# Kernel optimization log

Hardware: AMD Instinct MI355X
Metric: run time of the kernel (lower is better)

Reference implementation:

```python
import jax, jax.numpy as jnp
import numpy as np
from jax.scipy.special import logsumexp

T, B, D, L = 1024, 32, 768, 48
NEG = jnp.float32(-1e20)


def setup_inputs() -> dict:
    key = jax.random.key(0)
    ks = jax.random.split(key, 10)
    feats = jax.random.normal(ks[0], (T, B, D), jnp.float32)
    # tags: True = label disallowed at this position (partial annotation mask)
    tags = jax.random.uniform(ks[1], (T, B, L)) < 0.3
    lens = jax.random.randint(ks[2], (B,), T // 2, T + 1)
    W = jax.random.normal(ks[3], (D, L), jnp.float32) * 0.02
    b = jnp.zeros((L,), jnp.float32)
    base = jnp.float32(1.0 / L)
    begin_transition = jnp.full((L,), base) + 0.01 * jax.random.normal(ks[4], (L,), jnp.float32)
    transitions = jnp.full((L, L), base) + 0.01 * jax.random.normal(ks[5], (L, L), jnp.float32)
    end_transition = jnp.full((L,), base) + 0.01 * jax.random.normal(ks[6], (L,), jnp.float32)
    begin_constraints = jax.random.uniform(ks[7], (L,)) < 0.2
    end_constraints = jax.random.uniform(ks[8], (L,)) < 0.2
    transition_constraints = jax.random.uniform(ks[9], (L, L)) < 0.2
    return {
        "feats": feats, "tags": tags, "lens": lens,
        "W": W, "b": b,
        "begin_transition": begin_transition, "transitions": transitions,
        "end_transition": end_transition,
        "begin_constraints": begin_constraints, "end_constraints": end_constraints,
        "transition_constraints": transition_constraints,
    }


def _crf_logZ(emissions, begin, trans, end, tag_mask, lens):
    """Forward algorithm over [T,B,L] emissions; tag_mask True = disallowed.
    Returns log partition per batch element, read out at step lens-1."""
    fs0 = emissions[0] + begin[None, :]              # [B, L]
    fs0 = jnp.where(tag_mask[0], NEG, fs0)

    def step(prev, xs):
        em_t, m_t = xs
        # new[b, j] = logsumexp_k(prev[b, k] + trans[j, k]) + em_t[b, j]
        new = logsumexp(prev[:, None, :] + trans[None, :, :], axis=-1) + em_t
        new = jnp.where(m_t, NEG, new)
        return new, new

    _, ys = jax.lax.scan(step, fs0, (emissions[1:], tag_mask[1:]))
    all_fs = jnp.concatenate([fs0[None], ys], axis=0)        # [T, B, L]
    last = all_fs[lens - 1, jnp.arange(lens.shape[0])]       # [B, L]
    return logsumexp(last + end[None, :], axis=-1)           # [B]


def reference(feats, tags, lens, W, b, begin_transition, transitions,
              end_transition, begin_constraints, end_constraints,
              transition_constraints):
    # feature2labels (Dropout is identity in eval)
    emissions = jnp.einsum('tbd,dl->tbl', feats, W) + b      # [T, B, L]
    no_mask = jnp.zeros_like(tags)

    # forward_alg: unconstrained partition function
    fwd = _crf_logZ(emissions, begin_transition, transitions,
                    end_transition, no_mask, lens)

    # partial_score: constrained params + gold tag masking
    begin_m = jnp.where(begin_constraints, NEG, begin_transition)
    trans_m = jnp.where(transition_constraints, NEG, transitions)
    end_m = jnp.where(end_constraints, NEG, end_transition)
    par = _crf_logZ(emissions, begin_m, trans_m, end_m, tags, lens)

    # criterion per batch element (sum over batch = original scalar loss)
    return fwd - par                                          # [B]
```

## Files before the change

kernel.cpp:

```cpp
#include <hip/hip_runtime.h>

#define T_ 1024
#define B_ 32
#define D_ 768
#define L_ 48
#define TB_ (T_ * B_)

typedef __attribute__((ext_vector_type(4))) float f32x4;

__global__ __launch_bounds__(256) void emis_gemm(
    const float* __restrict__ feats, const float* __restrict__ W,
    const float* __restrict__ bias, float* __restrict__ E) {
  __shared__ float fbuf[128 * 64];
  __shared__ float wbuf[48 * 68];
  const int tid = threadIdx.x;
  const int wv = tid >> 6;
  const int lane = tid & 63;
  const int cg = tid & 7;
  const int rg = tid >> 3;
  const int c0 = cg * 6;
  const int rowbase = blockIdx.x * 128;
  const int r7 = rg & 7;

  float acc[4][6];
#pragma unroll
  for (int i = 0; i < 4; i++)
#pragma unroll
    for (int c = 0; c < 6; c++) acc[i][c] = 0.f;

  for (int kc = 0; kc < D_; kc += 64) {
    __syncthreads();

#pragma unroll
    for (int inst = 0; inst < 8; inst++) {
      const int rowstart = wv * 32 + inst * 4;
      const int r = rowstart + (lane >> 4);
      const int slot = lane & 15;
      const int gch = slot ^ (r & 7);
      const float* g = feats + (size_t)(rowbase + r) * D_ + kc + gch * 4;
      float* l = fbuf + rowstart * 64;
      __builtin_amdgcn_global_load_lds(
          (const __attribute__((address_space(1))) uint32_t*)g,
          (__attribute__((address_space(3))) uint32_t*)l, 16, 0, 0);
    }

#pragma unroll
    for (int i = 0; i < 12; i++) {
      const int idx = tid + i * 256;
      const int ko = idx / 48;
      const int j = idx - ko * 48;
      wbuf[j * 68 + ko] = W[(kc + ko) * L_ + j];
    }

    __syncthreads();

#pragma unroll 4
    for (int k4 = 0; k4 < 16; k4++) {
      float4 fv[4];
      float4 wv4[6];
      const int sch = (k4 ^ r7) << 2;
#pragma unroll
      for (int i = 0; i < 4; i++)
        fv[i] = *(const float4*)(fbuf + (rg + 32 * i) * 64 + sch);
#pragma unroll
      for (int c = 0; c < 6; c++)
        wv4[c] = *(const float4*)(wbuf + (c0 + c) * 68 + k4 * 4);
#pragma unroll
      for (int i = 0; i < 4; i++) {
#pragma unroll
        for (int c = 0; c < 6; c++) {
          acc[i][c] = fmaf(fv[i].x, wv4[c].x, acc[i][c]);
          acc[i][c] = fmaf(fv[i].y, wv4[c].y, acc[i][c]);
          acc[i][c] = fmaf(fv[i].z, wv4[c].z, acc[i][c]);
          acc[i][c] = fmaf(fv[i].w, wv4[c].w, acc[i][c]);
        }
      }
    }
  }

#pragma unroll
  for (int i = 0; i < 4; i++) {
    float* dst = E + (size_t)(rowbase + rg + 32 * i) * L_ + c0;
#pragma unroll
    for (int c = 0; c < 6; c += 2) {
      float2 v;
      v.x = __expf(acc[i][c + 0] + bias[c0 + c + 0]);
      v.y = __expf(acc[i][c + 1] + bias[c0 + c + 1]);
      *(float2*)(dst + c) = v;
    }
  }
}

__global__ __launch_bounds__(128) void crf_scan(
    const float* __restrict__ E, const int* __restrict__ tags,
    const int* __restrict__ lens, const float* __restrict__ begin,
    const float* __restrict__ trans, const float* __restrict__ endt,
    const int* __restrict__ bc, const int* __restrict__ ec,
    const int* __restrict__ tc, float* __restrict__ out) {
  __shared__ __align__(16) float sbuf[2][2][64];
  __shared__ float lzbuf[2];
  const int b = blockIdx.x;
  const int wv = threadIdx.x >> 6;
  const int lane = threadIdx.x & 63;
  const bool act = lane < L_;
  const bool par = (wv == 1);
  const int len = lens[b];
  const int stride = B_ * L_;
  const int base = b * L_ + (act ? lane : 0);

  float P[L_];
#pragma unroll
  for (int k = 0; k < L_; k++) P[k] = 0.f;
  if (act) {
#pragma unroll
    for (int k = 0; k < L_; k++) {
      float v = __expf(trans[lane * L_ + k]);
      if (par && tc[lane * L_ + k]) v = 0.f;
      P[k] = v;
    }
  }

  float a = 0.f;
  if (act) {
    a = E[base] * __expf(begin[lane]);
    if (par && (bc[lane] || tags[base])) a = 0.f;
  }
  float logacc = 0.f;
  float pend = 1.f;

  sbuf[wv][0][lane] = a;

  auto step = [&](int i, float ev, int tg, bool resc) {
    const float evp = ev * pend;
    pend = 1.f;
    const f32x4* src = (const f32x4*)sbuf[wv][i & 1];
    float s0 = 0.f, s1 = 0.f, s2 = 0.f, s3 = 0.f;
#pragma unroll
    for (int c = 0; c < 12; c++) {
      const f32x4 q = src[c];
      s0 = fmaf(q.x, P[4 * c + 0], s0);
      s1 = fmaf(q.y, P[4 * c + 1], s1);
      s2 = fmaf(q.z, P[4 * c + 2], s2);
      s3 = fmaf(q.w, P[4 * c + 3], s3);
    }
    float u = ((s0 + s1) + (s2 + s3)) * evp;
    if (tg) u = 0.f;
    a = u;
    sbuf[wv][(i + 1) & 1][lane] = u;
    if (resc) {
      float m = u;
#pragma unroll
      for (int off = 32; off; off >>= 1) m = fmaxf(m, __shfl_xor(m, off, 64));
      m = fmaxf(m, 1e-30f);
      logacc += __logf(m);
      pend = 1.f / m;
    }
  };

  float e8[8];
  int tg8[8];
#pragma unroll
  for (int i = 0; i < 8; i++) {
    e8[i] = E[(size_t)(1 + i) * stride + base];
    tg8[i] = par ? tags[(size_t)(1 + i) * stride + base] : 0;
  }

  int t = 1;
  for (; t + 8 <= len; t += 8) {
    float p8[8];
    int q8[8];
#pragma unroll
    for (int i = 0; i < 8; i++) {
      int tt = t + 8 + i;
      tt = (tt < len) ? tt : (len - 1);
      p8[i] = E[(size_t)tt * stride + base];
      q8[i] = par ? tags[(size_t)tt * stride + base] : 0;
    }
#pragma unroll
    for (int i = 0; i < 8; i++) step(i, e8[i], tg8[i], i == 7);
#pragma unroll
    for (int i = 0; i < 8; i++) { e8[i] = p8[i]; tg8[i] = q8[i]; }
  }
#pragma unroll
  for (int i = 0; i < 8; i++) {
    if (t + i < len) step(i, e8[i], tg8[i], false);
  }

  float z = 0.f;
  if (act) {
    float ez = __expf(endt[lane]);
    if (par && ec[lane]) ez = 0.f;
    z = a * ez;
  }
#pragma unroll
  for (int off = 32; off; off >>= 1) z += __shfl_xor(z, off, 64);
  if (lane == 0) lzbuf[wv] = logacc + __logf(pend) + __logf(z);
  __syncthreads();
  if (threadIdx.x == 0) out[b] = lzbuf[0] - lzbuf[1];
}

extern "C" void kernel_launch(void* const* d_in, const int* in_sizes, int n_in,
                              void* d_out, int out_size, void* d_ws,
                              size_t ws_size, hipStream_t stream) {
  (void)in_sizes; (void)n_in; (void)out_size; (void)ws_size;
  const float* feats = (const float*)d_in[0];
  const int* tags = (const int*)d_in[1];
  const int* lens = (const int*)d_in[2];
  const float* W = (const float*)d_in[3];
  const float* bias = (const float*)d_in[4];
  const float* begin = (const float*)d_in[5];
  const float* trans = (const float*)d_in[6];
  const float* endt = (const float*)d_in[7];
  const int* bc = (const int*)d_in[8];
  const int* ec = (const int*)d_in[9];
  const int* tc = (const int*)d_in[10];

  float* E = (float*)d_ws;
  float* out = (float*)d_out;

  emis_gemm<<<dim3(TB_ / 128), dim3(256), 0, stream>>>(feats, W, bias, E);
  crf_scan<<<dim3(B_), dim3(128), 0, stream>>>(E, tags, lens, begin, trans,
                                               endt, bc, ec, tc, out);
}
```

Measured before the change: 494.6 us.

## Double-buffer GEMM tiles and compute CRF rescale max from LDS without shuffles

The emission GEMM now double-buffers the feats and W tiles in LDS, prefetching the next k-chunk while computing the current one, so only one barrier per chunk remains. In the CRF scan, the rescale max is taken from the shared state vector already read during the matvec, which removes the cross-lane shuffle reduction from the serial dependency chain. The unroll drops from 8 to 4 steps with a rescale every 8 steps. LDS use doubles and the rescale now normalizes by the previous state's max instead of the new one, which changes numerics slightly.

```diff
diff --git a/kernel.cpp b/kernel.cpp
--- a/kernel.cpp
+++ b/kernel.cpp
@@ -8,11 +8,11 @@
 
 typedef __attribute__((ext_vector_type(4))) float f32x4;
 
-__global__ __launch_bounds__(256) void emis_gemm(
+__global__ __launch_bounds__(256, 1) void emis_gemm(
     const float* __restrict__ feats, const float* __restrict__ W,
     const float* __restrict__ bias, float* __restrict__ E) {
-  __shared__ float fbuf[128 * 64];
-  __shared__ float wbuf[48 * 68];
+  __shared__ float fbuf[2][128 * 64];
+  __shared__ float wbuf[2][48 * 68];
   const int tid = threadIdx.x;
   const int wv = tid >> 6;
   const int lane = tid & 63;
@@ -21,6 +21,17 @@
   const int c0 = cg * 6;
   const int rowbase = blockIdx.x * 128;
   const int r7 = rg & 7;
+  const int r_in = lane >> 4;
+  const int slot = lane & 15;
+
+  int woff[12];
+#pragma unroll
+  for (int i = 0; i < 12; i++) {
+    const int idx = tid + i * 256;
+    const int ko = idx / 48;
+    const int j = idx - ko * 48;
+    woff[i] = j * 68 + ko;
+  }
 
   float acc[4][6];
 #pragma unroll
@@ -28,32 +39,49 @@
 #pragma unroll
     for (int c = 0; c < 6; c++) acc[i][c] = 0.f;
 
-  for (int kc = 0; kc < D_; kc += 64) {
-    __syncthreads();
-
+  float wr[12];
+
+  {
+#pragma unroll
+    for (int i = 0; i < 12; i++) wr[i] = W[tid + i * 256];
 #pragma unroll
     for (int inst = 0; inst < 8; inst++) {
       const int rowstart = wv * 32 + inst * 4;
-      const int r = rowstart + (lane >> 4);
-      const int slot = lane & 15;
+      const int r = rowstart + r_in;
       const int gch = slot ^ (r & 7);
-      const float* g = feats + (size_t)(rowbase + r) * D_ + kc + gch * 4;
-      float* l = fbuf + rowstart * 64;
+      const float* g = feats + (size_t)(rowbase + r) * D_ + gch * 4;
+      float* l = &fbuf[0][rowstart * 64];
       __builtin_amdgcn_global_load_lds(
           (const __attribute__((address_space(1))) uint32_t*)g,
           (__attribute__((address_space(3))) uint32_t*)l, 16, 0, 0);
     }
-
-#pragma unroll
-    for (int i = 0; i < 12; i++) {
-      const int idx = tid + i * 256;
-      const int ko = idx / 48;
-      const int j = idx - ko * 48;
-      wbuf[j * 68 + ko] = W[(kc + ko) * L_ + j];
-    }
-
+#pragma unroll
+    for (int i = 0; i < 12; i++) wbuf[0][woff[i]] = wr[i];
+  }
+
+  for (int c = 0; c < 12; c++) {
+    const int cur = c & 1;
     __syncthreads();
 
+    if (c < 11) {
+      const int kc2 = (c + 1) * 64;
+#pragma unroll
+      for (int i = 0; i < 12; i++) wr[i] = W[kc2 * L_ + tid + i * 256];
+#pragma unroll
+      for (int inst = 0; inst < 8; inst++) {
+        const int rowstart = wv * 32 + inst * 4;
+        const int r = rowstart + r_in;
+        const int gch = slot ^ (r & 7);
+        const float* g = feats + (size_t)(rowbase + r) * D_ + kc2 + gch * 4;
+        float* l = &fbuf[cur ^ 1][rowstart * 64];
+        __builtin_amdgcn_global_load_lds(
+            (const __attribute__((address_space(1))) uint32_t*)g,
+            (__attribute__((address_space(3))) uint32_t*)l, 16, 0, 0);
+      }
+    }
+
+    const float* fb = fbuf[cur];
+    const float* wb = wbuf[cur];
 #pragma unroll 4
     for (int k4 = 0; k4 < 16; k4++) {
       float4 fv[4];
@@ -61,37 +89,42 @@
       const int sch = (k4 ^ r7) << 2;
 #pragma unroll
       for (int i = 0; i < 4; i++)
-        fv[i] = *(const float4*)(fbuf + (rg + 32 * i) * 64 + sch);
-#pragma unroll
-      for (int c = 0; c < 6; c++)
-        wv4[c] = *(const float4*)(wbuf + (c0 + c) * 68 + k4 * 4);
+        fv[i] = *(const float4*)(fb + (rg + 32 * i) * 64 + sch);
+#pragma unroll
+      for (int cc = 0; cc < 6; cc++)
+        wv4[cc] = *(const float4*)(wb + (c0 + cc) * 68 + k4 * 4);
 #pragma unroll
       for (int i = 0; i < 4; i++) {
 #pragma unroll
-        for (int c = 0; c < 6; c++) {
-          acc[i][c] = fmaf(fv[i].x, wv4[c].x, acc[i][c]);
-          acc[i][c] = fmaf(fv[i].y, wv4[c].y, acc[i][c]);
-          acc[i][c] = fmaf(fv[i].z, wv4[c].z, acc[i][c]);
-          acc[i][c] = fmaf(fv[i].w, wv4[c].w, acc[i][c]);
+        for (int cc = 0; cc < 6; cc++) {
+          acc[i][cc] = fmaf(fv[i].x, wv4[cc].x, acc[i][cc]);
+          acc[i][cc] = fmaf(fv[i].y, wv4[cc].y, acc[i][cc]);
+          acc[i][cc] = fmaf(fv[i].z, wv4[cc].z, acc[i][cc]);
+          acc[i][cc] = fmaf(fv[i].w, wv4[cc].w, acc[i][cc]);
         }
       }
     }
+
+    if (c < 11) {
+#pragma unroll
+      for (int i = 0; i < 12; i++) wbuf[cur ^ 1][woff[i]] = wr[i];
+    }
   }
 
 #pragma unroll
   for (int i = 0; i < 4; i++) {
     float* dst = E + (size_t)(rowbase + rg + 32 * i) * L_ + c0;
 #pragma unroll
-    for (int c = 0; c < 6; c += 2) {
+    for (int cc = 0; cc < 6; cc += 2) {
       float2 v;
-      v.x = __expf(acc[i][c + 0] + bias[c0 + c + 0]);
-      v.y = __expf(acc[i][c + 1] + bias[c0 + c + 1]);
-      *(float2*)(dst + c) = v;
+      v.x = __expf(acc[i][cc + 0] + bias[c0 + cc + 0]);
+      v.y = __expf(acc[i][cc + 1] + bias[c0 + cc + 1]);
+      *(float2*)(dst + cc) = v;
     }
   }
 }
 
-__global__ __launch_bounds__(128) void crf_scan(
+__global__ __launch_bounds__(128, 1) void crf_scan(
     const float* __restrict__ E, const int* __restrict__ tags,
     const int* __restrict__ lens, const float* __restrict__ begin,
     const float* __restrict__ trans, const float* __restrict__ endt,
@@ -126,64 +159,73 @@
     if (par && (bc[lane] || tags[base])) a = 0.f;
   }
   float logacc = 0.f;
-  float pend = 1.f;
 
   sbuf[wv][0][lane] = a;
 
   auto step = [&](int i, float ev, int tg, bool resc) {
-    const float evp = ev * pend;
-    pend = 1.f;
     const f32x4* src = (const f32x4*)sbuf[wv][i & 1];
     float s0 = 0.f, s1 = 0.f, s2 = 0.f, s3 = 0.f;
+    f32x4 mx = {0.f, 0.f, 0.f, 0.f};
 #pragma unroll
     for (int c = 0; c < 12; c++) {
       const f32x4 q = src[c];
+      if (resc) {
+        mx.x = fmaxf(mx.x, q.x);
+        mx.y = fmaxf(mx.y, q.y);
+        mx.z = fmaxf(mx.z, q.z);
+        mx.w = fmaxf(mx.w, q.w);
+      }
       s0 = fmaf(q.x, P[4 * c + 0], s0);
       s1 = fmaf(q.y, P[4 * c + 1], s1);
       s2 = fmaf(q.z, P[4 * c + 2], s2);
       s3 = fmaf(q.w, P[4 * c + 3], s3);
     }
+    float evp = ev;
+    if (resc) {
+      float m = fmaxf(fmaxf(mx.x, mx.y), fmaxf(mx.z, mx.w));
+      m = fmaxf(m, 1e-30f);
+      logacc += __logf(m);
+      evp = ev * (1.f / m);
+    }
     float u = ((s0 + s1) + (s2 + s3)) * evp;
     if (tg) u = 0.f;
     a = u;
     sbuf[wv][(i + 1) & 1][lane] = u;
-    if (resc) {
-      float m = u;
-#pragma unroll
-      for (int off = 32; off; off >>= 1) m = fmaxf(m, __shfl_xor(m, off, 64));
-      m = fmaxf(m, 1e-30f);
-      logacc += __logf(m);
-      pend = 1.f / m;
-    }
   };
 
-  float e8[8];
-  int tg8[8];
-#pragma unroll
-  for (int i = 0; i < 8; i++) {
-    e8[i] = E[(size_t)(1 + i) * stride + base];
-    tg8[i] = par ? tags[(size_t)(1 + i) * stride + base] : 0;
+  float e4[4];
+  int tg4[4];
+#pragma unroll
+  for (int i = 0; i < 4; i++) {
+    e4[i] = E[(size_t)(1 + i) * stride + base];
+    tg4[i] = par ? tags[(size_t)(1 + i) * stride + base] : 0;
   }
 
   int t = 1;
-  for (; t + 8 <= len; t += 8) {
-    float p8[8];
-    int q8[8];
-#pragma unroll
-    for (int i = 0; i < 8; i++) {
-      int tt = t + 8 + i;
+  for (; t + 4 <= len; t += 4) {
+    float p4[4];
+    int q4[4];
+#pragma unroll
+    for (int i = 0; i < 4; i++) {
+      int tt = t + 4 + i;
       tt = (tt < len) ? tt : (len - 1);
-      p8[i] = E[(size_t)tt * stride + base];
-      q8[i] = par ? tags[(size_t)tt * stride + base] : 0;
-    }
-#pragma unroll
-    for (int i = 0; i < 8; i++) step(i, e8[i], tg8[i], i == 7);
-#pragma unroll
-    for (int i = 0; i < 8; i++) { e8[i] = p8[i]; tg8[i] = q8[i]; }
-  }
-#pragma unroll
-  for (int i = 0; i < 8; i++) {
-    if (t + i < len) step(i, e8[i], tg8[i], false);
+      p4[i] = E[(size_t)tt * stride + base];
+      q4[i] = par ? tags[(size_t)tt * stride + base] : 0;
+    }
+    if ((t & 7) == 1) {
+      step(0, e4[0], tg4[0], true);
+    } else {
+      step(0, e4[0], tg4[0], false);
+    }
+    step(1, e4[1], tg4[1], false);
+    step(2, e4[2], tg4[2], false);
+    step(3, e4[3], tg4[3], false);
+#pragma unroll
+    for (int i = 0; i < 4; i++) { e4[i] = p4[i]; tg4[i] = q4[i]; }
+  }
+#pragma unroll
+  for (int i = 0; i < 4; i++) {
+    if (t + i < len) step(i, e4[i], tg4[i], false);
   }
 
   float z = 0.f;
@@ -194,7 +236,7 @@
   }
 #pragma unroll
   for (int off = 32; off; off >>= 1) z += __shfl_xor(z, off, 64);
-  if (lane == 0) lzbuf[wv] = logacc + __logf(pend) + __logf(z);
+  if (lane == 0) lzbuf[wv] = logacc + __logf(z);
   __syncthreads();
   if (threadIdx.x == 0) out[b] = lzbuf[0] - lzbuf[1];
 }
```

Result: faster. 446.7 us (-9.7%).
